# Kernel optimization log

Hardware: AMD Instinct MI355X
Metric: run time of the kernel (lower is better)

Reference implementation:

```python
import jax, jax.numpy as jnp
import numpy as np

B, S, D, H = 16, 1024, 768, 12
HS = D // H  # head size = 64
NEG = -1000000.0  # module uses -1e6, not -inf


def setup_inputs() -> dict:
    key = jax.random.key(0)
    k1, k2, k3 = jax.random.split(key, 3)
    scale = 1.0 / np.sqrt(D)
    return {
        "x": jax.random.normal(k1, (B, S, D), dtype=jnp.float32),
        "W_qkv": jax.random.normal(k2, (D, 3 * D), dtype=jnp.float32) * scale,
        "b_qkv": jnp.zeros((3 * D,), dtype=jnp.float32),
        "W_o": jax.random.normal(k3, (D, D), dtype=jnp.float32) * scale,
        "b_o": jnp.zeros((D,), dtype=jnp.float32),
    }


def reference(x, W_qkv, b_qkv, W_o, b_o):
    qkv = x @ W_qkv + b_qkv                      # [B,S,3D]
    q, k, v = jnp.split(qkv, 3, axis=-1)         # each [B,S,D]
    q = q.reshape(B, S, H, HS)
    k = k.reshape(B, S, H, HS)
    v = v.reshape(B, S, H, HS)
    scores = jnp.einsum('bqhd,bkhd->bhqk', q, k) / np.sqrt(HS).astype(np.float32)
    causal = jnp.tril(jnp.ones((S, S), dtype=bool))
    scores = jnp.where(causal, scores, jnp.float32(NEG))
    probs = jax.nn.softmax(scores, axis=-1)      # dropout is eval-mode identity
    av = jnp.einsum('bhqk,bkhd->bqhd', probs, v).reshape(B, S, D)
    return av @ W_o + b_o
```

## Files before the change

kernel.cpp:

```cpp
#include <hip/hip_runtime.h>
#include <stdint.h>

typedef unsigned short u16;
typedef __attribute__((ext_vector_type(8))) short bf16x8;
typedef __attribute__((ext_vector_type(8))) u16 u16x8;
typedef __attribute__((ext_vector_type(4))) u16 u16x4;
typedef __attribute__((ext_vector_type(4))) float f32x4;
typedef __attribute__((ext_vector_type(16))) float f32x16;

#define B_ 16
#define S_ 1024
#define D_ 768
#define H_ 12

__device__ __forceinline__ float bf2f(u16 u) {
  unsigned int x = ((unsigned int)u) << 16;
  float f;
  __builtin_memcpy(&f, &x, 4);
  return f;
}
__device__ __forceinline__ u16 f2bf(float f) {
  unsigned int x;
  __builtin_memcpy(&x, &f, 4);
  x += 0x7fffu + ((x >> 16) & 1u);
  return (u16)(x >> 16);
}

#define MFMA16(a, b, c) __builtin_amdgcn_mfma_f32_16x16x32_bf16((a), (b), (c), 0, 0, 0)
#define MFMA32(a, b, c) __builtin_amdgcn_mfma_f32_32x32x16_bf16((a), (b), (c), 0, 0, 0)

#define GLD16(g, l)                                              \
  __builtin_amdgcn_global_load_lds(                              \
      (const __attribute__((address_space(1))) void*)(g),        \
      (__attribute__((address_space(3))) void*)(l), 16, 0, 0)

__global__ __launch_bounds__(256) void cvt_bf16(const float* __restrict__ in,
                                                u16* __restrict__ out, int n8) {
  const int i = blockIdx.x * 256 + threadIdx.x;
  if (i >= n8) return;
  const float4 a = *(const float4*)(in + (size_t)i * 8);
  const float4 b = *(const float4*)(in + (size_t)i * 8 + 4);
  u16x8 o;
  o[0] = f2bf(a.x); o[1] = f2bf(a.y); o[2] = f2bf(a.z); o[3] = f2bf(a.w);
  o[4] = f2bf(b.x); o[5] = f2bf(b.y); o[6] = f2bf(b.z); o[7] = f2bf(b.w);
  *(u16x8*)(out + (size_t)i * 8) = o;
}

__global__ __launch_bounds__(256) void transpose_cvt(const float* __restrict__ W,
                                                     u16* __restrict__ Wt, int K, int N) {
  __shared__ u16 t[32][33];
  const int n0 = blockIdx.x * 32, k0 = blockIdx.y * 32;
  const int tx = threadIdx.x & 31, ty = threadIdx.x >> 5;
#pragma unroll
  for (int i = 0; i < 32; i += 8)
    t[ty + i][tx] = f2bf(W[(size_t)(k0 + ty + i) * N + n0 + tx]);
  __syncthreads();
#pragma unroll
  for (int i = 0; i < 32; i += 8) Wt[(size_t)(n0 + ty + i) * K + k0 + tx] = t[tx][ty + i];
}

template <int MODE>
__global__ __launch_bounds__(256) void gemm_bt(const u16* __restrict__ A,
                                               const u16* __restrict__ Bt,
                                               const float* __restrict__ bias,
                                               u16* __restrict__ O0, u16* __restrict__ O1,
                                               u16* __restrict__ O2, float* __restrict__ Of,
                                               int M, int N, int K) {
  __shared__ u16 Al[2 * 128 * 32];
  __shared__ u16 Bl[2 * 128 * 32];
  const int tid = threadIdx.x;
  const int wid = tid >> 6, lane = tid & 63;
  const int lo = lane & 15, hi = lane >> 4;
  const int wr = wid >> 1, wc = wid & 1;
  const int m0 = blockIdx.x * 128, n0 = blockIdx.y * 128;
  const int rA = lane >> 2;
  const int kc = (lane & 3) * 8;
  const int srow = wid * 16 + rA;
  f32x4 acc[4][4] = {};
  const int kiters = K >> 5;

  GLD16(A + (size_t)(m0 + srow) * K + kc, (char*)Al + wid * 1024);
  GLD16(A + (size_t)(m0 + srow + 64) * K + kc, (char*)Al + 4096 + wid * 1024);
  GLD16(Bt + (size_t)(n0 + srow) * K + kc, (char*)Bl + wid * 1024);
  GLD16(Bt + (size_t)(n0 + srow + 64) * K + kc, (char*)Bl + 4096 + wid * 1024);
  asm volatile("s_waitcnt vmcnt(0)" ::: "memory");
  __builtin_amdgcn_s_barrier();

  int cur = 0;
  for (int kt = 0; kt < kiters; ++kt) {
    if (kt + 1 < kiters) {
      const int k0 = (kt + 1) * 32;
      const int nb = (cur ^ 1) * 8192;
      GLD16(A + (size_t)(m0 + srow) * K + k0 + kc, (char*)Al + nb + wid * 1024);
      GLD16(A + (size_t)(m0 + srow + 64) * K + k0 + kc, (char*)Al + nb + 4096 + wid * 1024);
      GLD16(Bt + (size_t)(n0 + srow) * K + k0 + kc, (char*)Bl + nb + wid * 1024);
      GLD16(Bt + (size_t)(n0 + srow + 64) * K + k0 + kc, (char*)Bl + nb + 4096 + wid * 1024);
    }
    const int cb = cur * 4096;
    bf16x8 af[4], bfr[4];
#pragma unroll
    for (int i = 0; i < 4; ++i)
      af[i] = *(const bf16x8*)&Al[cb + (wr * 64 + i * 16 + lo) * 32 + hi * 8];
#pragma unroll
    for (int j = 0; j < 4; ++j)
      bfr[j] = *(const bf16x8*)&Bl[cb + (wc * 64 + j * 16 + lo) * 32 + hi * 8];
    __builtin_amdgcn_s_setprio(1);
#pragma unroll
    for (int i = 0; i < 4; ++i)
#pragma unroll
      for (int j = 0; j < 4; ++j) acc[i][j] = MFMA16(af[i], bfr[j], acc[i][j]);
    __builtin_amdgcn_s_setprio(0);
    asm volatile("s_waitcnt vmcnt(0)" ::: "memory");
    __builtin_amdgcn_s_barrier();
    cur ^= 1;
  }
#pragma unroll
  for (int j = 0; j < 4; ++j) {
    const int n = n0 + wc * 64 + j * 16 + lo;
    const float bv = bias[n];
#pragma unroll
    for (int i = 0; i < 4; ++i) {
#pragma unroll
      for (int r = 0; r < 4; ++r) {
        const int m = m0 + wr * 64 + i * 16 + hi * 4 + r;
        const float fv = acc[i][j][r] + bv;
        if (MODE == 0) {
          const u16 o = f2bf(fv);
          if (n0 < D_) {
            O0[(size_t)m * D_ + n] = o;
          } else if (n0 < 2 * D_) {
            O1[(size_t)m * D_ + (n - D_)] = o;
          } else {
            const int np = n - 2 * D_;
            O2[(((size_t)(m >> 10) * H_ + (np >> 6)) * 64 + (np & 63)) * S_ + (m & 1023)] = o;
          }
        } else {
          Of[(size_t)m * N + n] = fv;
        }
      }
    }
  }
}

__global__ __launch_bounds__(256) void attn_fwd2(const u16* __restrict__ Qb,
                                                 const u16* __restrict__ Kb,
                                                 const u16* __restrict__ VTb,
                                                 u16* __restrict__ att) {
  __shared__ u16 Kl[2048];
  __shared__ u16 Vl[2048];
  const int tid = threadIdx.x;
  const int lane = tid & 63, wid = tid >> 6;
  const int l31 = lane & 31, hi1 = lane >> 5;
  const int L = blockIdx.x + 8 * (blockIdx.y + 12 * blockIdx.z);
  const int bx = (L >> 3) & 7;
  const int P = (L & 7) + 8 * (L >> 6);
  const int h = P % 12, b = P / 12;
  const int q0 = bx * 128;
  const int qw0 = q0 + wid * 32;
  const int qg = qw0 + l31;
  const size_t rowbase = (size_t)b * S_;

  bf16x8 qf[4];
  {
    const u16* qp = Qb + (rowbase + qg) * D_ + h * 64 + hi1 * 8;
#pragma unroll
    for (int c = 0; c < 4; ++c) {
      bf16x8 v = *(const bf16x8*)(qp + c * 16);
#pragma unroll
      for (int j = 0; j < 8; ++j) v[j] = (short)f2bf(bf2f((u16)v[j]) * 0.125f);
      qf[c] = v;
    }
  }
  float mrun = -3.0e38f, lrun = 0.0f;
  f32x16 o0 = {}, o1 = {};

  const u16* kgp =
      Kb + (rowbase + (tid & 31)) * D_ + h * 64 + (tid >> 6) * 16 + ((tid >> 5) & 1) * 8;
  const u16* vgp = VTb +
                   (((size_t)b * H_ + h) * 64 + ((tid >> 6) & 1) * 32 + (tid & 31)) * S_ +
                   (tid >> 7) * 16 + ((tid >> 5) & 1) * 8;
  char* kdst = (char*)Kl + wid * 1024;
  char* vdst = (char*)Vl + wid * 1024;
  const char* kbase = (const char*)Kl + lane * 16;
  const char* vbase = (const char*)Vl + lane * 16;

  const int kvend = q0 + 128;
  for (int kv0 = 0; kv0 < kvend; kv0 += 32) {
    __syncthreads();
    GLD16(kgp + (size_t)kv0 * D_, kdst);
    GLD16(vgp + kv0, vdst);
    __syncthreads();
    if (kv0 > qw0 + 31) continue;

    f32x16 s = {};
#pragma unroll
    for (int c = 0; c < 4; ++c) s = MFMA32(*(const bf16x8*)(kbase + c * 1024), qf[c], s);

    if (kv0 + 31 > qw0) {
#pragma unroll
      for (int r = 0; r < 16; ++r) {
        const int kvg = kv0 + (r & 3) + 8 * (r >> 2) + 4 * hi1;
        if (kvg > qg) s[r] = -1.0e30f;
      }
    }
    float rm = s[0];
#pragma unroll
    for (int r = 1; r < 16; ++r) rm = fmaxf(rm, s[r]);
    rm = fmaxf(rm, __shfl_xor(rm, 32));
    const float mn = fmaxf(mrun, rm);
    const float fr = __expf(mrun - mn);
    mrun = mn;
    float p[16];
    float rs = 0.0f;
#pragma unroll
    for (int r = 0; r < 16; ++r) {
      p[r] = __expf(s[r] - mn);
      rs += p[r];
    }
    rs += __shfl_xor(rs, 32);
    lrun = lrun * fr + rs;
#pragma unroll
    for (int r = 0; r < 16; ++r) {
      o0[r] *= fr;
      o1[r] *= fr;
    }
    unsigned int pa[4], pb[4];
#pragma unroll
    for (int g = 0; g < 4; ++g) {
      pa[g] = (unsigned)f2bf(p[4 * g]) | ((unsigned)f2bf(p[4 * g + 1]) << 16);
      pb[g] = (unsigned)f2bf(p[4 * g + 2]) | ((unsigned)f2bf(p[4 * g + 3]) << 16);
    }
    const unsigned sa = __shfl_xor(hi1 ? pa[0] : pa[1], 32);
    const unsigned sb = __shfl_xor(hi1 ? pb[0] : pb[1], 32);
    const unsigned sc = __shfl_xor(hi1 ? pa[2] : pa[3], 32);
    const unsigned sd = __shfl_xor(hi1 ? pb[2] : pb[3], 32);
    const uint4 w0 = hi1 ? make_uint4(sa, sb, pa[1], pb[1]) : make_uint4(pa[0], pb[0], sa, sb);
    const uint4 w1 = hi1 ? make_uint4(sc, sd, pa[3], pb[3]) : make_uint4(pa[2], pb[2], sc, sd);
    bf16x8 pf0, pf1;
    __builtin_memcpy(&pf0, &w0, 16);
    __builtin_memcpy(&pf1, &w1, 16);
    o0 = MFMA32(*(const bf16x8*)(vbase + 0 * 1024), pf0, o0);
    o1 = MFMA32(*(const bf16x8*)(vbase + 1 * 1024), pf0, o1);
    o0 = MFMA32(*(const bf16x8*)(vbase + 2 * 1024), pf1, o0);
    o1 = MFMA32(*(const bf16x8*)(vbase + 3 * 1024), pf1, o1);
  }
  const float inv = 1.0f / lrun;
  u16* op = att + (rowbase + qg) * D_ + h * 64;
#pragma unroll
  for (int g = 0; g < 4; ++g) {
    u16x4 v0, v1;
#pragma unroll
    for (int j = 0; j < 4; ++j) {
      v0[j] = f2bf(o0[4 * g + j] * inv);
      v1[j] = f2bf(o1[4 * g + j] * inv);
    }
    *(u16x4*)(op + 8 * g + 4 * hi1) = v0;
    *(u16x4*)(op + 32 + 8 * g + 4 * hi1) = v1;
  }
}

extern "C" void kernel_launch(void* const* d_in, const int* in_sizes, int n_in, void* d_out,
                              int out_size, void* d_ws, size_t ws_size, hipStream_t stream) {
  const float *x = nullptr, *Wqkv = nullptr, *bqkv = nullptr, *Wo = nullptr, *bo = nullptr;
  for (int i = 0; i < n_in; ++i) {
    switch (in_sizes[i]) {
      case 16384 * 768:  x = (const float*)d_in[i]; break;
      case 768 * 2304:   Wqkv = (const float*)d_in[i]; break;
      case 2304:         bqkv = (const float*)d_in[i]; break;
      case 768 * 768:    Wo = (const float*)d_in[i]; break;
      case 768:          bo = (const float*)d_in[i]; break;
    }
  }
  float* out = (float*)d_out;

  char* ws = (char*)d_ws;
  u16* WqkvT = (u16*)(ws);
  u16* WoT = (u16*)(ws + 3538944);
  u16* Qb = (u16*)(ws + 4718592);
  u16* Kb = (u16*)(ws + 29884416);
  u16* VT = (u16*)(ws + 55050240);
  u16* xb = (u16*)d_out;
  u16* att = Qb;

  cvt_bf16<<<(16384 * 768 / 8 + 255) / 256, 256, 0, stream>>>(x, xb, 16384 * 768 / 8);
  transpose_cvt<<<dim3(2304 / 32, 768 / 32), 256, 0, stream>>>(Wqkv, WqkvT, 768, 2304);
  transpose_cvt<<<dim3(768 / 32, 768 / 32), 256, 0, stream>>>(Wo, WoT, 768, 768);
  gemm_bt<0><<<dim3(16384 / 128, 2304 / 128), 256, 0, stream>>>(
      xb, WqkvT, bqkv, Qb, Kb, VT, nullptr, 16384, 2304, 768);
  attn_fwd2<<<dim3(8, H_, B_), 256, 0, stream>>>(Qb, Kb, VT, att);
  gemm_bt<1><<<dim3(16384 / 128, 768 / 128), 256, 0, stream>>>(
      att, WoT, bo, nullptr, nullptr, nullptr, out, 16384, 768, 768);
}
```

Before: 251.9 us.

## Triple-buffer GEMM LDS staging with two-tile prefetch and partial vmcnt waits

Raises the shared-memory ring for the A and B tiles in the bf16 GEMM from two buffers to three and prefetches two K-tiles ahead. The wait now uses vmcnt(4), so only the older stage has to land and one stage's global loads stay in flight across the barrier. The aim is to hide global-load latency better in the QKV and output projection GEMMs. The cost is 50% more LDS per block, which may reduce occupancy, plus a modulo-3 index in the loop.

```diff
diff --git a/kernel.cpp b/kernel.cpp
--- a/kernel.cpp
+++ b/kernel.cpp
@@ -66,8 +66,8 @@
                                                u16* __restrict__ O0, u16* __restrict__ O1,
                                                u16* __restrict__ O2, float* __restrict__ Of,
                                                int M, int N, int K) {
-  __shared__ u16 Al[2 * 128 * 32];
-  __shared__ u16 Bl[2 * 128 * 32];
+  __shared__ u16 Al[3 * 128 * 32];
+  __shared__ u16 Bl[3 * 128 * 32];
   const int tid = threadIdx.x;
   const int wid = tid >> 6, lane = tid & 63;
   const int lo = lane & 15, hi = lane >> 4;
@@ -79,24 +79,31 @@
   f32x4 acc[4][4] = {};
   const int kiters = K >> 5;
 
-  GLD16(A + (size_t)(m0 + srow) * K + kc, (char*)Al + wid * 1024);
-  GLD16(A + (size_t)(m0 + srow + 64) * K + kc, (char*)Al + 4096 + wid * 1024);
-  GLD16(Bt + (size_t)(n0 + srow) * K + kc, (char*)Bl + wid * 1024);
-  GLD16(Bt + (size_t)(n0 + srow + 64) * K + kc, (char*)Bl + 4096 + wid * 1024);
-  asm volatile("s_waitcnt vmcnt(0)" ::: "memory");
+  const u16* agp0 = A + (size_t)(m0 + srow) * K + kc;
+  const u16* agp1 = A + (size_t)(m0 + srow + 64) * K + kc;
+  const u16* bgp0 = Bt + (size_t)(n0 + srow) * K + kc;
+  const u16* bgp1 = Bt + (size_t)(n0 + srow + 64) * K + kc;
+  const int wb = wid * 1024;
+
+#define STAGE(kt, buf)                                          \
+  do {                                                          \
+    const int _k0 = (kt) * 32;                                  \
+    const int _nb = (buf) * 8192;    \
+    GLD16(agp0 + _k0, (char*)Al + _nb + wb);                    \
+    GLD16(agp1 + _k0, (char*)Al + _nb + 4096 + wb);             \
+    GLD16(bgp0 + _k0, (char*)Bl + _nb + wb);                    \
+    GLD16(bgp1 + _k0, (char*)Bl + _nb + 4096 + wb);             \
+  } while (0)
+
+  STAGE(0, 0);
+  STAGE(1, 1);
+  asm volatile("s_waitcnt vmcnt(4)" ::: "memory");
   __builtin_amdgcn_s_barrier();
 
-  int cur = 0;
   for (int kt = 0; kt < kiters; ++kt) {
-    if (kt + 1 < kiters) {
-      const int k0 = (kt + 1) * 32;
-      const int nb = (cur ^ 1) * 8192;
-      GLD16(A + (size_t)(m0 + srow) * K + k0 + kc, (char*)Al + nb + wid * 1024);
-      GLD16(A + (size_t)(m0 + srow + 64) * K + k0 + kc, (char*)Al + nb + 4096 + wid * 1024);
-      GLD16(Bt + (size_t)(n0 + srow) * K + k0 + kc, (char*)Bl + nb + wid * 1024);
-      GLD16(Bt + (size_t)(n0 + srow + 64) * K + k0 + kc, (char*)Bl + nb + 4096 + wid * 1024);
-    }
-    const int cb = cur * 4096;
+    const bool st = (kt + 2 < kiters);
+    if (st) STAGE(kt + 2, (kt + 2) % 3);
+    const int cb = (kt % 3) * 4096;
     bf16x8 af[4], bfr[4];
 #pragma unroll
     for (int i = 0; i < 4; ++i)
@@ -110,10 +117,14 @@
 #pragma unroll
       for (int j = 0; j < 4; ++j) acc[i][j] = MFMA16(af[i], bfr[j], acc[i][j]);
     __builtin_amdgcn_s_setprio(0);
-    asm volatile("s_waitcnt vmcnt(0)" ::: "memory");
+    if (st) {
+      asm volatile("s_waitcnt vmcnt(4)" ::: "memory");
+    } else if (kt + 1 < kiters) {
+      asm volatile("s_waitcnt vmcnt(0)" ::: "memory");
+    }
     __builtin_amdgcn_s_barrier();
-    cur ^= 1;
-  }
+  }
+#undef STAGE
 #pragma unroll
   for (int j = 0; j < 4; ++j) {
     const int n = n0 + wc * 64 + j * 16 + lo;
```

Result: no change. 254.2 us (+0.9%).
